# Kernel optimization log

Hardware: AMD Instinct MI355X
Metric: run time of the kernel (lower is better)

Reference implementation:

```python
import jax, jax.numpy as jnp
import numpy as np

NEG = -1e30   # safe -inf surrogate
EPS = 1e-7    # keras.backend.epsilon() used by ctc_batch_cost


def setup_inputs() -> dict:
    key = jax.random.key(0)
    k1, k2 = jax.random.split(key)
    B, T, C, L = 512, 512, 256, 64
    u = jax.random.uniform(k1, (B, T, C), dtype=jnp.float32, minval=1e-3, maxval=1.0)
    y_pred = u / jnp.sum(u, axis=-1, keepdims=True)  # softmax-like probabilities
    y_true = jax.random.randint(k2, (B, L), 0, C - 1)  # labels in [0, C-2]; blank = C-1
    return {"y_true": y_true, "y_pred": y_pred}


def ctc_loss(y_true, y_pred):
    # Faithful to K.ctc_batch_cost with label_length = L, input_length = T for all samples.
    B, T, C = y_pred.shape
    L = y_true.shape[1]
    S = 2 * L + 1            # extended label length (blanks interleaved)
    blank = C - 1            # TF CTC convention: blank is last class
    labels = y_true.astype(jnp.int32)

    # extended labels: [blank, l1, blank, l2, ..., lL, blank]
    ext = jnp.full((B, S), blank, dtype=jnp.int32).at[:, 1::2].set(labels)
    prev2 = jnp.concatenate([jnp.full((B, 2), blank, jnp.int32), ext[:, :-2]], axis=1)
    # transition s-2 -> s allowed only for non-blank states with ext[s] != ext[s-2]
    skip = (ext != blank) & (ext != prev2)

    logp = jnp.log(y_pred + EPS)                                   # [B,T,C]
    idx = jnp.broadcast_to(ext[:, None, :], (B, T, S))
    lp_ext = jnp.take_along_axis(logp, idx, axis=2)                # [B,T,S]

    # alpha at t=0: only states 0 (blank) and 1 (first label) reachable
    alpha0 = jnp.full((B, S), NEG, dtype=logp.dtype)
    alpha0 = alpha0.at[:, 0].set(lp_ext[:, 0, 0]).at[:, 1].set(lp_ext[:, 0, 1])

    def step(alpha, lp_t):
        a1 = jnp.concatenate([jnp.full((B, 1), NEG, alpha.dtype), alpha[:, :-1]], axis=1)
        a2 = jnp.concatenate([jnp.full((B, 2), NEG, alpha.dtype), alpha[:, :-2]], axis=1)
        m = jnp.logaddexp(jnp.logaddexp(alpha, a1), jnp.where(skip, a2, NEG))
        return m + lp_t, None

    lp_seq = jnp.transpose(lp_ext, (1, 0, 2))[1:]                  # [T-1,B,S]
    alphaT, _ = jax.lax.scan(step, alpha0, lp_seq)

    # total log-likelihood ends in last blank or last label
    loss = -jnp.logaddexp(alphaT[:, S - 1], alphaT[:, S - 2])      # [B]
    return loss[:, None]                                           # [B,1] like ctc_batch_cost


def reference(y_true, y_pred):
    return ctc_loss(y_true, y_pred)
```

## Files before the change

kernel.cpp:

```cpp
#include <hip/hip_runtime.h>


#define NEGF (-1e30f)
#define EPSF (1e-7f)

constexpr int T_ = 512;
constexpr int C_ = 256;
constexpr int L_ = 64;
constexpr int NBUF = 16;

__device__ __forceinline__ float lae2(float a, float b) {
    float m = fmaxf(a, b);
    float d = fminf(a, b) - m;
    return m + __logf(1.0f + __expf(d));
}

__global__ __launch_bounds__(64, 1)
void ctc_kernel(const int* __restrict__ y_true,
                const float* __restrict__ y_pred,
                float* __restrict__ out) {
    const int b    = blockIdx.x;
    const int lane = threadIdx.x;
    const int blank = C_ - 1;

    const int* lab = y_true + b * L_;
    const int e1    = lab[lane];
    const int eprev = (lane == 0) ? blank : lab[lane - 1];
    const bool skip1 = (e1 != blank) && (e1 != eprev);

    const float* row = y_pred + (size_t)b * T_ * C_;

    float pb[NBUF];
    float pl[NBUF];
#pragma unroll
    for (int j = 0; j < NBUF; ++j) {
        pb[j] = row[j * C_ + blank];
        pl[j] = row[j * C_ + e1];
    }

    float a0 = NEGF;
    float a1 = NEGF;
    float a2 = NEGF;

    for (int t0 = 0; t0 < T_; t0 += NBUF) {
#pragma unroll
        for (int j = 0; j < NBUF; ++j) {
            const int t = t0 + j;
            const float lp0 = __logf(pb[j] + EPSF);
            const float lp1 = __logf(pl[j] + EPSF);

            int tn = t + NBUF;
            if (tn > T_ - 1) tn = T_ - 1;
            pb[j] = row[tn * C_ + blank];
            pl[j] = row[tn * C_ + e1];

            if (t == 0) {
                a0 = (lane == 0) ? lp0 : NEGF;
                a1 = (lane == 0) ? lp1 : NEGF;
                a2 = NEGF;
            } else {
                float pa1 = __shfl_up(a1, 1, 64);
                if (lane == 0) pa1 = NEGF;

                const float na0 = lae2(a0, pa1) + lp0;

                const float c3 = skip1 ? pa1 : NEGF;
                const float m  = fmaxf(fmaxf(a1, a0), c3);
                const float s  = __expf(a1 - m) + __expf(a0 - m) + __expf(c3 - m);
                const float na1 = m + __logf(s) + lp1;

                const float na2 = lae2(a2, a1) + lp0;

                a0 = na0; a1 = na1; a2 = na2;
            }
        }
    }

    if (lane == 63) {
        out[b] = -lae2(a1, a2);
    }
}

extern "C" void kernel_launch(void* const* d_in, const int* in_sizes, int n_in,
                              void* d_out, int out_size, void* d_ws, size_t ws_size,
                              hipStream_t stream) {
    const int*   y_true = (const int*)d_in[0];
    const float* y_pred = (const float*)d_in[1];
    float*       out    = (float*)d_out;

    const int B = in_sizes[0] / L_;
    ctc_kernel<<<dim3(B), dim3(64), 0, stream>>>(y_true, y_pred, out);
}
```

Baseline: 418.8 us.

## Stream y_pred rows into an LDS ring via async global_load_lds prefetch

Each wave now copies whole time-step rows of y_pred into a 64-row LDS ring buffer with coalesced asynchronous global-to-LDS loads, keeping three 16-row chunks in flight. Waits are controlled by explicit s_waitcnt on the vector-memory counter. The recurrence then reads the blank and label probabilities from LDS, and the logs are computed eight steps ahead in a register ring. The neighbour shift is also changed from __shfl_up to a DPP row-shift. This aims to hide global-memory latency in the serial time loop, at the cost of moving the full C-wide rows rather than only the two needed values per step, plus 64 KB of LDS per block.

```diff
diff --git a/kernel.cpp b/kernel.cpp
--- a/kernel.cpp
+++ b/kernel.cpp
@@ -4,10 +4,13 @@
 #define NEGF (-1e30f)
 #define EPSF (1e-7f)
 
-constexpr int T_ = 512;
-constexpr int C_ = 256;
-constexpr int L_ = 64;
-constexpr int NBUF = 16;
+constexpr int T_   = 512;
+constexpr int C_   = 256;
+constexpr int L_   = 64;
+constexpr int TCH  = 16;
+constexpr int NCH  = T_ / TCH;
+constexpr int NROW = 64;
+constexpr int PD   = 8;
 
 __device__ __forceinline__ float lae2(float a, float b) {
     float m = fmaxf(a, b);
@@ -15,51 +18,89 @@
     return m + __logf(1.0f + __expf(d));
 }
 
+__device__ __forceinline__ float wave_shr1(float x) {
+    int r = __builtin_amdgcn_update_dpp(0, __float_as_int(x),
+                                        0x138 ,
+                                        0xF, 0xF, true );
+    return __int_as_float(r);
+}
+
+typedef const __attribute__((address_space(1))) void GV;
+typedef __attribute__((address_space(3))) void LV;
+
 __global__ __launch_bounds__(64, 1)
 void ctc_kernel(const int* __restrict__ y_true,
                 const float* __restrict__ y_pred,
                 float* __restrict__ out) {
-    const int b    = blockIdx.x;
-    const int lane = threadIdx.x;
+    __shared__ float tile[NROW * C_];
+
+    const int b     = blockIdx.x;
+    const int lane  = threadIdx.x;
     const int blank = C_ - 1;
 
-    const int* lab = y_true + b * L_;
+    const int* lab  = y_true + b * L_;
     const int e1    = lab[lane];
     const int eprev = (lane == 0) ? blank : lab[lane - 1];
     const bool skip1 = (e1 != blank) && (e1 != eprev);
 
-    const float* row = y_pred + (size_t)b * T_ * C_;
+    const float* __restrict__ row = y_pred + (size_t)b * T_ * C_;
 
-    float pb[NBUF];
-    float pl[NBUF];
+    auto issue_chunk = [&](int c) {
+        const float* src = row + (size_t)c * TCH * C_ + lane * 4;
+        float* dst = &tile[((c * TCH) & (NROW - 1)) * C_];
 #pragma unroll
-    for (int j = 0; j < NBUF; ++j) {
-        pb[j] = row[j * C_ + blank];
-        pl[j] = row[j * C_ + e1];
+        for (int r = 0; r < TCH; ++r) {
+            __builtin_amdgcn_global_load_lds((GV*)(src + r * C_),
+                                             (LV*)(dst + r * C_),
+                                             16, 0, 0);
+        }
+    };
+
+    issue_chunk(0); issue_chunk(1); issue_chunk(2); issue_chunk(3);
+    __builtin_amdgcn_s_waitcnt(0x8F70);
+
+    float plp0[PD], plp1[PD];
+#pragma unroll
+    for (int j = 0; j < PD; ++j) {
+        float p0 = tile[j * C_ + blank];
+        float p1 = tile[j * C_ + e1];
+        plp0[j] = __logf(p0 + EPSF);
+        plp1[j] = __logf(p1 + EPSF);
     }
 
-    float a0 = NEGF;
-    float a1 = NEGF;
-    float a2 = NEGF;
+    float a0 = NEGF, a1 = NEGF, a2 = NEGF;
 
-    for (int t0 = 0; t0 < T_; t0 += NBUF) {
+    for (int c = 0; c < NCH; ++c) {
+        if (c > 0) {
+            const int cn = c + 3;
+            if (cn < NCH) {
+                issue_chunk(cn);
+                __builtin_amdgcn_s_waitcnt(0x8F70);
+            } else if (c + 2 < NCH) {
+                __builtin_amdgcn_s_waitcnt(0x4F70);
+            } else {
+                __builtin_amdgcn_s_waitcnt(0x0F70);
+            }
+        }
 #pragma unroll
-        for (int j = 0; j < NBUF; ++j) {
-            const int t = t0 + j;
-            const float lp0 = __logf(pb[j] + EPSF);
-            const float lp1 = __logf(pl[j] + EPSF);
+        for (int j = 0; j < TCH; ++j) {
+            const int t = c * TCH + j;
+            const float lp0 = plp0[j & (PD - 1)];
+            const float lp1 = plp1[j & (PD - 1)];
 
-            int tn = t + NBUF;
-            if (tn > T_ - 1) tn = T_ - 1;
-            pb[j] = row[tn * C_ + blank];
-            pl[j] = row[tn * C_ + e1];
+            int tn = t + PD; if (tn > T_ - 1) tn = T_ - 1;
+            const int rbase = (tn & (NROW - 1)) * C_;
+            const float q0 = tile[rbase + blank];
+            const float q1 = tile[rbase + e1];
+            plp0[j & (PD - 1)] = __logf(q0 + EPSF);
+            plp1[j & (PD - 1)] = __logf(q1 + EPSF);
 
-            if (t == 0) {
+            if (c == 0 && j == 0) {
                 a0 = (lane == 0) ? lp0 : NEGF;
                 a1 = (lane == 0) ? lp1 : NEGF;
                 a2 = NEGF;
             } else {
-                float pa1 = __shfl_up(a1, 1, 64);
+                float pa1 = wave_shr1(a1);
                 if (lane == 0) pa1 = NEGF;
 
                 const float na0 = lae2(a0, pa1) + lp0;
```

Result: faster. 402.1 us (-4.0%).
